# Kernel optimization log

Measured on AMD Instinct MI355X. Metric: run time of the kernel, lower is better.

Reference implementation:

```python
import jax, jax.numpy as jnp
import numpy as np

DIM = 96          # model dim (channels)
DS = 16           # d_state
K = 4             # d_conv
DIN = 2 * DIM     # d_inner = expand * dim
DTR = 6           # dt_rank = ceil(dim/16)
NSLICES = 4
B, H, W, Z = 2, 24, 24, 24
L = H * W * Z


def layernorm(x, g, b):
    mu = jnp.mean(x, -1, keepdims=True)
    var = jnp.var(x, -1, keepdims=True)
    return (x - mu) * jax.lax.rsqrt(var + 1e-5) * g + b


def dwconv_causal(x, w, b):
    # x: (B,L,Din), w: (Din,K) depthwise causal conv, b: (Din,)
    xt = x.swapaxes(1, 2)  # (B,Din,L)
    y = jax.lax.conv_general_dilated(xt, w[:, None, :], (1,), [(K - 1, 0)],
                                     feature_group_count=w.shape[0])
    return (y + b[None, :, None]).swapaxes(1, 2)


def selective_scan(u, dt, Bc, Cc, A, Dp):
    # u,dt: (B,L,Din); Bc,Cc: (B,L,DS); A: (Din,DS); Dp: (Din,)
    def step(h, inp):
        u_t, dt_t, B_t, C_t = inp
        dA = jnp.exp(dt_t[..., None] * A)                       # (B,Din,DS)
        h = dA * h + (dt_t * u_t)[..., None] * B_t[:, None, :]  # (B,Din,DS)
        y = jnp.sum(h * C_t[:, None, :], -1)                    # (B,Din)
        return h, y
    h0 = jnp.zeros((u.shape[0], u.shape[2], A.shape[1]), u.dtype)
    xs = (u.swapaxes(0, 1), dt.swapaxes(0, 1), Bc.swapaxes(0, 1), Cc.swapaxes(0, 1))
    _, ys = jax.lax.scan(step, h0, xs)
    return ys.swapaxes(0, 1) + u * Dp


def conv3d(x, w, b):
    y = jax.lax.conv_general_dilated(x, w, (1, 1, 1), [(1, 1), (1, 1), (1, 1)],
                                     dimension_numbers=('NCDHW', 'OIDHW', 'NCDHW'))
    return y + b[None, :, None, None, None]


def _slice_perm(t):  # group tokens by residue mod NSLICES (inter-slice scan)
    b, l, d = t.shape
    return t.reshape(b, l // NSLICES, NSLICES, d).transpose(0, 2, 1, 3).reshape(b, l, d)


def _slice_inv(t):
    b, l, d = t.shape
    return t.reshape(b, NSLICES, l // NSLICES, d).transpose(0, 2, 1, 3).reshape(b, l, d)


def setup_inputs() -> dict:
    key = jax.random.key(0)
    ks = jax.random.split(key, 10)
    r = lambda k, shp, s=0.02: jax.random.normal(k, shp, jnp.float32) * s
    return {
        'x': jax.random.normal(ks[0], (B, DIM, H, W, Z), jnp.float32),
        'ln_g': jnp.ones((DIM,), jnp.float32),
        'ln_b': jnp.zeros((DIM,), jnp.float32),
        'in_proj_w': r(ks[1], (2 * DIN, DIM)),
        'conv_w': r(ks[2], (3, DIN, K), 0.1),
        'conv_b': jnp.zeros((3, DIN), jnp.float32),
        'xproj_w': r(ks[3], (3, DTR + 2 * DS, DIN)),
        'dt_w': r(ks[4], (3, DIN, DTR), 0.1),
        'dt_b': jnp.full((3, DIN), -2.0, jnp.float32),
        'A_log': jnp.tile(jnp.log(jnp.arange(1, DS + 1, dtype=jnp.float32))[None, None, :], (3, DIN, 1)),
        'Dp': jnp.ones((3, DIN), jnp.float32),
        'out_proj_w': r(ks[5], (DIM, DIN)),
        'f1_w': r(ks[6], (DIM, 2 * DIM, 3, 3, 3)),
        'f1_b': jnp.zeros((DIM,), jnp.float32),
        'f2_w': r(ks[7], (DIM, 2 * DIM, 3, 3, 3)),
        'f2_b': jnp.zeros((DIM,), jnp.float32),
    }


def _mfa_forward(x, ln_g, ln_b, in_proj_w, conv_w, conv_b, xproj_w, dt_w, dt_b,
                 A_log, Dp, out_proj_w, f1_w, f1_b, f2_w, f2_b):
    b, c, h, w, z = x.shape
    l = h * w * z
    x_flat = x.reshape(b, c, l).swapaxes(1, 2)            # (B,L,C)
    x_norm = layernorm(x_flat, ln_g, ln_b)
    xz = x_norm @ in_proj_w.T                              # (B,L,2*Din)
    xin, zg = jnp.split(xz, [DIN], axis=-1)
    gate = jax.nn.silu(zg)

    ident = lambda t: t
    flip = lambda t: t[:, ::-1]
    perms = [(ident, ident), (flip, flip), (_slice_perm, _slice_inv)]

    ys = []
    for i, (fwd_p, inv_p) in enumerate(perms):
        xb = fwd_p(xin)
        u = jax.nn.silu(dwconv_causal(xb, conv_w[i], conv_b[i]))
        xdbl = u @ xproj_w[i].T                            # (B,L,DTR+2*DS)
        dtr, Bc, Cc = jnp.split(xdbl, [DTR, DTR + DS], axis=-1)
        dt = jax.nn.softplus(dtr @ dt_w[i].T + dt_b[i])
        y = selective_scan(u, dt, Bc, Cc, -jnp.exp(A_log[i]), Dp[i])
        ys.append(inv_p(y) * gate)
    q, k, v = ys                                           # each (B,L,Din)
    out = (q + k + v) @ out_proj_w.T                       # (B,L,C)

    # channel cross-covariance attention (head dim of 1 squeezed out)
    attn = jax.nn.softmax(jnp.einsum('bld,ble->bde', q, k), -1)   # (B,Din,Din)
    out_a = jnp.einsum('bld,bed->ble', v, attn)                   # v @ attn^T, (B,L,Din)
    out_a = out_a.reshape(b, 2 * c, h, w, z)                      # torch .view semantics (row-major)
    out_a = conv3d(out_a, f1_w, f1_b)
    out_m = out.swapaxes(1, 2).reshape(b, c, h, w, z)
    out2 = conv3d(jnp.concatenate([out_a, out_m], axis=1), f2_w, f2_b)
    return out2 + x


def reference(x, ln_g, ln_b, in_proj_w, conv_w, conv_b, xproj_w, dt_w, dt_b,
              A_log, Dp, out_proj_w, f1_w, f1_b, f2_w, f2_b):
    return _mfa_forward(x, ln_g, ln_b, in_proj_w, conv_w, conv_b, xproj_w, dt_w,
                        dt_b, A_log, Dp, out_proj_w, f1_w, f1_b, f2_w, f2_b)
```

## Files before the change

### kernel.cpp

```cpp
#include <hip/hip_runtime.h>
#include <hip/hip_bf16.h>
#include <math.h>

#define BB 2
#define C0 96
#define LTOT 13824
#define DINC 192
#define L4S 3456
#define NCHUNK 216
#define CLEN 64

#define WS_FLOATS 92000000
__device__ __attribute__((aligned(256))) float g_ws[WS_FLOATS];

typedef __bf16 bf16x8 __attribute__((ext_vector_type(8)));
typedef short  s16x8  __attribute__((ext_vector_type(8)));
typedef short  s16x4  __attribute__((ext_vector_type(4)));
typedef float  f32x4  __attribute__((ext_vector_type(4)));

__device__ __forceinline__ f32x4 mfma16(s16x8 a, s16x8 b, f32x4 c){
  return __builtin_amdgcn_mfma_f32_16x16x32_bf16(
      __builtin_bit_cast(bf16x8, a), __builtin_bit_cast(bf16x8, b), c, 0, 0, 0);
}

__device__ __forceinline__ int sigma_idx(int dir, int p){
  if (dir == 0) return p;
  if (dir == 1) return LTOT - 1 - p;
  return 4*(p % L4S) + (p / L4S);
}

__device__ __forceinline__ float silu_f(float x){
  return x / (1.f + __expf(-x));
}

__device__ __forceinline__ float softplus_f(float x){
  return (x > 20.f) ? x : __logf(1.f + __expf(x));
}

__device__ __forceinline__ short bf16r(float x){
  return (short)__builtin_bit_cast(unsigned short, __float2bfloat16(x));
}

__device__ __forceinline__ void pow_tree(float e1, float* pw){
  pw[0] = e1;
  pw[1] = e1*e1;
  pw[2] = pw[1]*e1;
  pw[3] = pw[1]*pw[1];
  pw[4] = pw[3]*e1;
  pw[5] = pw[3]*pw[1];
  pw[6] = pw[3]*pw[2];
  pw[7] = pw[3]*pw[3];
  pw[8] = pw[7]*e1;
  pw[9] = pw[7]*pw[1];
  pw[10]= pw[7]*pw[2];
  pw[11]= pw[7]*pw[3];
  pw[12]= pw[7]*pw[4];
  pw[13]= pw[7]*pw[5];
  pw[14]= pw[7]*pw[6];
  pw[15]= pw[7]*pw[7];
}

__global__ __launch_bounds__(256) void k_ln(const float* __restrict__ x,
    const float* __restrict__ g, const float* __restrict__ bt, float* __restrict__ xn)
{
  int i = blockIdx.x*256 + threadIdx.x;
  if (i >= BB*LTOT) return;
  int b = i / LTOT, ll = i % LTOT;
  const float* xp = x + (size_t)b*C0*LTOT + ll;
  float s = 0.f, ss = 0.f;
  for (int c = 0; c < C0; ++c){ float v = xp[(size_t)c*LTOT]; s += v; ss += v*v; }
  float mu = s * (1.f/C0);
  float var = ss * (1.f/C0) - mu*mu;
  float inv = rsqrtf(var + 1e-5f);
  float* op = xn + (size_t)i*C0;
  for (int c = 0; c < C0; ++c){
    float v = xp[(size_t)c*LTOT];
    op[c] = (v - mu)*inv*g[c] + bt[c];
  }
}

__global__ __launch_bounds__(256) void k_inproj(const float* __restrict__ xnorm,
    const float* __restrict__ W, float* __restrict__ xin, float* __restrict__ gate)
{
  __shared__ short Qs[256][40];
  __shared__ short Ws[96][40];
  int tid = threadIdx.x;
  long row0 = (long)blockIdx.x * 256;
  int y = blockIdx.y;
  int colb = (y & 1)*96;
  bool isGate = (y >= 2);
  const float* Wp = W + (long)y*96*96;
  int lane = tid & 63, wid = tid >> 6;
  int lr = lane & 15, lk = lane >> 4;
  f32x4 acc[4][6];
  #pragma unroll
  for (int i = 0; i < 4; ++i)
    #pragma unroll
    for (int j = 0; j < 6; ++j) acc[i][j] = f32x4{0.f,0.f,0.f,0.f};
  for (int kc = 0; kc < 3; ++kc){
    #pragma unroll
    for (int i = 0; i < 8; ++i){
      int flat4 = i*256 + tid;
      int row = flat4 >> 3, col4 = flat4 & 7;
      f32x4 a = *(const f32x4*)(xnorm + (row0 + row)*96 + kc*32 + col4*4);
      s16x4 o;
      #pragma unroll
      for (int e = 0; e < 4; ++e) o[e] = bf16r(a[e]);
      *(s16x4*)&Qs[row][col4*4] = o;
    }
    #pragma unroll
    for (int i = 0; i < 3; ++i){
      int flat4 = i*256 + tid;
      int row = flat4 >> 3, col4 = flat4 & 7;
      f32x4 wv = *(const f32x4*)(Wp + (long)row*96 + kc*32 + col4*4);
      s16x4 o;
      #pragma unroll
      for (int e = 0; e < 4; ++e) o[e] = bf16r(wv[e]);
      *(s16x4*)&Ws[row][col4*4] = o;
    }
    __syncthreads();
    #pragma unroll
    for (int rf = 0; rf < 4; ++rf){
      s16x8 af = *(const s16x8*)&Qs[wid*64 + rf*16 + lr][lk*8];
      #pragma unroll
      for (int cf = 0; cf < 6; ++cf){
        s16x8 wf = *(const s16x8*)&Ws[cf*16 + lr][lk*8];
        acc[rf][cf] = mfma16(wf, af, acc[rf][cf]);
      }
    }
    __syncthreads();
  }
  float* dst = isGate ? gate : xin;
  #pragma unroll
  for (int rf = 0; rf < 4; ++rf)
    #pragma unroll
    for (int cf = 0; cf < 6; ++cf){
      long l = row0 + wid*64 + rf*16 + lr;
      int n0 = cf*16 + lk*4;
      f32x4 v = acc[rf][cf];
      if (isGate){
        #pragma unroll
        for (int e = 0; e < 4; ++e) v[e] = silu_f(v[e]);
      }
      *(f32x4*)(dst + l*DINC + colb + n0) = v;
    }
}

__global__ __launch_bounds__(256) void k_xproj(const float* __restrict__ u,
    const float* __restrict__ W, float* __restrict__ xdbl)
{
  __shared__ short Qs[256][40];
  __shared__ short Ws[48][40];
  int tid = threadIdx.x;
  long row0 = (long)blockIdx.x * 256;
  int dir = (int)(row0 / 27648);
  const float* Wp = W + (long)dir*38*192;
  int lane = tid & 63, wid = tid >> 6;
  int lr = lane & 15, lk = lane >> 4;
  f32x4 acc[4][3];
  #pragma unroll
  for (int i = 0; i < 4; ++i)
    #pragma unroll
    for (int j = 0; j < 3; ++j) acc[i][j] = f32x4{0.f,0.f,0.f,0.f};
  for (int kc = 0; kc < 6; ++kc){
    #pragma unroll
    for (int i = 0; i < 8; ++i){
      int flat4 = i*256 + tid;
      int row = flat4 >> 3, col4 = flat4 & 7;
      f32x4 a = *(const f32x4*)(u + (row0 + row)*(long)DINC + kc*32 + col4*4);
      s16x4 o;
      #pragma unroll
      for (int e = 0; e < 4; ++e) o[e] = bf16r(a[e]);
      *(s16x4*)&Qs[row][col4*4] = o;
    }
    #pragma unroll
    for (int i = 0; i < 2; ++i){
      int flat4 = i*256 + tid;
      if (flat4 < 384){
        int row = flat4 >> 3, col4 = flat4 & 7;
        s16x4 o = {0,0,0,0};
        if (row < 38){
          f32x4 wv = *(const f32x4*)(Wp + (long)row*DINC + kc*32 + col4*4);
          #pragma unroll
          for (int e = 0; e < 4; ++e) o[e] = bf16r(wv[e]);
        }
        *(s16x4*)&Ws[row][col4*4] = o;
      }
    }
    __syncthreads();
    #pragma unroll
    for (int rf = 0; rf < 4; ++rf){
      s16x8 af = *(const s16x8*)&Qs[wid*64 + rf*16 + lr][lk*8];
      #pragma unroll
      for (int cf = 0; cf < 3; ++cf){
        s16x8 wf = *(const s16x8*)&Ws[cf*16 + lr][lk*8];
        acc[rf][cf] = mfma16(wf, af, acc[rf][cf]);
      }
    }
    __syncthreads();
  }
  #pragma unroll
  for (int rf = 0; rf < 4; ++rf)
    #pragma unroll
    for (int cf = 0; cf < 3; ++cf){
      long row = row0 + wid*64 + rf*16 + lr;
      int n0 = cf*16 + lk*4;
      if (n0 < 38)
        *(f32x4*)(xdbl + row*40 + n0) = acc[rf][cf];
    }
}

__global__ __launch_bounds__(256) void k_dwconv(const float* __restrict__ xin,
    const float* __restrict__ cw, const float* __restrict__ cb, float* __restrict__ u)
{
  long i = (long)blockIdx.x*256 + threadIdx.x;
  if (i >= 3L*BB*LTOT*48) return;
  int dq = (int)(i % 48); long t = i / 48;
  int p = (int)(t % LTOT); t /= LTOT;
  int b = (int)(t % BB); int dir = (int)(t / BB);
  int d0 = dq*4;
  f32x4 acc = *(const f32x4*)(cb + dir*DINC + d0);
  const float* wbase = cw + ((long)dir*DINC + d0)*4;
  f32x4 w0 = *(const f32x4*)(wbase);
  f32x4 w1 = *(const f32x4*)(wbase + 4);
  f32x4 w2 = *(const f32x4*)(wbase + 8);
  f32x4 w3 = *(const f32x4*)(wbase + 12);
  #pragma unroll
  for (int kk = 0; kk < 4; ++kk){
    int pp = p - 3 + kk;
    if (pp >= 0){
      int l = sigma_idx(dir, pp);
      f32x4 xv = *(const f32x4*)(xin + ((long)b*LTOT + l)*DINC + d0);
      acc[0] += xv[0] * w0[kk];
      acc[1] += xv[1] * w1[kk];
      acc[2] += xv[2] * w2[kk];
      acc[3] += xv[3] * w3[kk];
    }
  }
  #pragma unroll
  for (int e = 0; e < 4; ++e) acc[e] = silu_f(acc[e]);
  *(f32x4*)(u + (((long)dir*BB + b)*LTOT + p)*DINC + d0) = acc;
}

__global__ __launch_bounds__(256) void k_prepA(const float* __restrict__ al, float* __restrict__ A){
  int i = blockIdx.x*256 + threadIdx.x;
  if (i < 3*DINC*16) A[i] = -__expf(al[i]);
}

__global__ __launch_bounds__(192) void k_scan1(const float* __restrict__ u,
    const float* __restrict__ dt_w, const float* __restrict__ dt_b,
    const float* __restrict__ xdbl,
    const float* __restrict__ Abuf, float* __restrict__ aprod, float* __restrict__ hend)
{
  int d = threadIdx.x;
  int c  = blockIdx.x % NCHUNK;
  int bd = blockIdx.x / NCHUNK;
  int dir = bd >> 1;
  long pbase = (long)bd*LTOT + (long)c*CLEN;
  float w6[6];
  #pragma unroll
  for (int i = 0; i < 6; ++i) w6[i] = dt_w[(dir*DINC + d)*6 + i];
  float bdt = dt_b[dir*DINC + d];
  float A[16], h[16];
  #pragma unroll
  for (int s = 0; s < 16; ++s){
    A[s] = Abuf[((long)dir*DINC + d)*16 + s];
    h[s] = 0.f;
  }
  float A0 = A[0];
  bool fast = true;
  #pragma unroll
  for (int s = 1; s < 16; ++s)
    fast = fast && (fabsf(A[s] - (float)(s+1)*A0) <= 1e-4f*(float)(s+1));
  float sum_dt = 0.f;
  if (fast){
    for (int j = 0; j < CLEN; ++j){
      const float* xr = xdbl + (pbase + j)*40;
      float lu = u[(pbase + j)*DINC + d];
      float xv = bdt;
      #pragma unroll
      for (int i = 0; i < 6; ++i) xv += xr[i]*w6[i];
      float ldt = softplus_f(xv);
      sum_dt += ldt;
      float du = ldt*lu;
      float pw[16];
      pow_tree(__expf(ldt*A0), pw);
      #pragma unroll
      for (int s = 0; s < 16; ++s) h[s] = pw[s]*h[s] + du*xr[6+s];
    }
  } else {
    for (int j = 0; j < CLEN; ++j){
      const float* xr = xdbl + (pbase + j)*40;
      float lu = u[(pbase + j)*DINC + d];
      float xv = bdt;
      #pragma unroll
      for (int i = 0; i < 6; ++i) xv += xr[i]*w6[i];
      float ldt = softplus_f(xv);
      sum_dt += ldt;
      float du = ldt*lu;
      #pragma unroll
      for (int s = 0; s < 16; ++s) h[s] = __expf(ldt*A[s])*h[s] + du*xr[6+s];
    }
  }
  long oi = (((long)bd*DINC + d)*NCHUNK + c)*16;
  if (fast){
    float pw[16];
    pow_tree(__expf(A0*sum_dt), pw);
    #pragma unroll
    for (int s = 0; s < 16; ++s){ aprod[oi + s] = pw[s]; hend[oi + s] = h[s]; }
  } else {
    #pragma unroll
    for (int s = 0; s < 16; ++s){ aprod[oi + s] = __expf(A[s]*sum_dt); hend[oi + s] = h[s]; }
  }
}

__global__ __launch_bounds__(256) void k_scan2(float* __restrict__ aprod, const float* __restrict__ hend){
  long i = (long)blockIdx.x*256 + threadIdx.x;
  if (i >= 6L*DINC*16) return;
  int s = (int)(i & 15); long t = i >> 4;
  int d = (int)(t % DINC); int bd = (int)(t / DINC);
  long base = (((long)bd*DINC + d)*NCHUNK)*16 + s;
  float H = 0.f;
  for (int c = 0; c < NCHUNK; ++c){
    long idx = base + (long)c*16;
    float a = aprod[idx], he = hend[idx];
    aprod[idx] = H;
    H = he + a*H;
  }
}

__global__ __launch_bounds__(192) void k_scan3(const float* __restrict__ u,
    const float* __restrict__ dt_w, const float* __restrict__ dt_b,
    const float* __restrict__ xdbl,
    const float* __restrict__ Abuf, const float* __restrict__ hin,
    const float* __restrict__ Dp, const float* __restrict__ gate, float* __restrict__ qkv)
{
  int d = threadIdx.x;
  int c  = blockIdx.x % NCHUNK;
  int bd = blockIdx.x / NCHUNK;
  int dir = bd >> 1, b = bd & 1;
  long pbase = (long)bd*LTOT + (long)c*CLEN;
  float w6[6];
  #pragma unroll
  for (int i = 0; i < 6; ++i) w6[i] = dt_w[(dir*DINC + d)*6 + i];
  float bdt = dt_b[dir*DINC + d];
  float A[16], h[16];
  long oi = (((long)bd*DINC + d)*NCHUNK + c)*16;
  #pragma unroll
  for (int s = 0; s < 16; ++s){
    A[s] = Abuf[((long)dir*DINC + d)*16 + s];
    h[s] = hin[oi + s];
  }
  float A0 = A[0];
  bool fast = true;
  #pragma unroll
  for (int s = 1; s < 16; ++s)
    fast = fast && (fabsf(A[s] - (float)(s+1)*A0) <= 1e-4f*(float)(s+1));
  float Dv = Dp[dir*DINC + d];
  if (fast){
    for (int j = 0; j < CLEN; ++j){
      const float* xr = xdbl + (pbase + j)*40;
      float lu = u[(pbase + j)*DINC + d];
      float xv = bdt;
      #pragma unroll
      for (int i = 0; i < 6; ++i) xv += xr[i]*w6[i];
      float ldt = softplus_f(xv);
      float du = ldt*lu;
      float pw[16];
      pow_tree(__expf(ldt*A0), pw);
      float y = 0.f;
      #pragma unroll
      for (int s = 0; s < 16; ++s){
        h[s] = pw[s]*h[s] + du*xr[6+s];
        y += h[s]*xr[22+s];
      }
      int pl = c*CLEN + j;
      int l = sigma_idx(dir, pl);
      long li = (long)b*LTOT + l;
      qkv[(((long)dir*BB + b)*LTOT + l)*DINC + d] = (y + lu*Dv) * gate[li*DINC + d];
    }
  } else {
    for (int j = 0; j < CLEN; ++j){
      const float* xr = xdbl + (pbase + j)*40;
      float lu = u[(pbase + j)*DINC + d];
      float xv = bdt;
      #pragma unroll
      for (int i = 0; i < 6; ++i) xv += xr[i]*w6[i];
      float ldt = softplus_f(xv);
      float du = ldt*lu;
      float y = 0.f;
      #pragma unroll
      for (int s = 0; s < 16; ++s){
        h[s] = __expf(ldt*A[s])*h[s] + du*xr[6+s];
        y += h[s]*xr[22+s];
      }
      int pl = c*CLEN + j;
      int l = sigma_idx(dir, pl);
      long li = (long)b*LTOT + l;
      qkv[(((long)dir*BB + b)*LTOT + l)*DINC + d] = (y + lu*Dv) * gate[li*DINC + d];
    }
  }
}

__global__ __launch_bounds__(256) void k_zero(float* __restrict__ p, int n){
  int i = blockIdx.x*256 + threadIdx.x;
  if (i < n) p[i] = 0.f;
}

__global__ __launch_bounds__(256) void k_qk(const float* __restrict__ q,
    const float* __restrict__ k, float* __restrict__ attn)
{
  __shared__ float Qs[32][64];
  __shared__ float Ks[32][64];
  int tid = threadIdx.x;
  int bx = blockIdx.x;
  int lc = bx % 24; int et = (bx/24) % 3; int dtl = (bx/72) % 3; int b = bx/216;
  long base = (long)b*LTOT;
  int l0 = lc*576;
  float acc[4][4] = {};
  int col = tid & 63, rbase = tid >> 6;
  for (int ls = 0; ls < 576; ls += 32){
    #pragma unroll
    for (int rr = 0; rr < 8; ++rr){
      int r = rbase + rr*4;
      long l = base + l0 + ls + r;
      Qs[r][col] = q[l*DINC + dtl*64 + col];
      Ks[r][col] = k[l*DINC + et *64 + col];
    }
    __syncthreads();
    int d0 = (tid & 15)*4, e0 = (tid >> 4)*4;
    #pragma unroll
    for (int ll = 0; ll < 32; ++ll){
      float qa[4], ka[4];
      #pragma unroll
      for (int i = 0; i < 4; ++i){ qa[i] = Qs[ll][d0+i]; ka[i] = Ks[ll][e0+i]; }
      #pragma unroll
      for (int i = 0; i < 4; ++i)
        #pragma unroll
        for (int j = 0; j < 4; ++j) acc[i][j] += qa[i]*ka[j];
    }
    __syncthreads();
  }
  int d0 = (tid & 15)*4, e0 = (tid >> 4)*4;
  #pragma unroll
  for (int i = 0; i < 4; ++i)
    #pragma unroll
    for (int j = 0; j < 4; ++j)
      atomicAdd(&attn[((long)b*DINC + dtl*64 + d0 + i)*DINC + et*64 + e0 + j], acc[i][j]);
}

__global__ __launch_bounds__(64) void k_softmax(float* __restrict__ attn){
  int row = blockIdx.x, tid = threadIdx.x;
  float* p = attn + (long)row*DINC;
  float v0 = p[tid], v1 = p[tid+64], v2 = p[tid+128];
  float m = fmaxf(v0, fmaxf(v1, v2));
  #pragma unroll
  for (int off = 32; off >= 1; off >>= 1) m = fmaxf(m, __shfl_xor(m, off));
  float e0 = __expf(v0-m), e1 = __expf(v1-m), e2 = __expf(v2-m);
  float s = e0 + e1 + e2;
  #pragma unroll
  for (int off = 32; off >= 1; off >>= 1) s += __shfl_xor(s, off);
  float inv = 1.f/s;
  p[tid] = e0*inv; p[tid+64] = e1*inv; p[tid+128] = e2*inv;
}

__global__ __launch_bounds__(256) void k_outa(const float* __restrict__ v,
    const float* __restrict__ attn, __hip_bfloat16* __restrict__ inT1)
{
  __shared__ short Vs[192][40];
  __shared__ short Ws[192][40];
  int tid = threadIdx.x;
  int r0 = blockIdx.x;
  int b  = blockIdx.y;
  int lane = tid & 63, wid = tid >> 6;
  int lr = lane & 15, lk = lane >> 4;
  const float* vb = v + (long)b*LTOT*DINC;
  const float* ab = attn + (long)b*DINC*DINC;
  f32x4 acc[3][12];
  #pragma unroll
  for (int i = 0; i < 3; ++i)
    #pragma unroll
    for (int j = 0; j < 12; ++j) acc[i][j] = f32x4{0.f,0.f,0.f,0.f};
  for (int kc = 0; kc < 6; ++kc){
    #pragma unroll
    for (int i = 0; i < 6; ++i){
      int flat4 = i*256 + tid;
      int row = flat4 >> 3, col4 = flat4 & 7;
      int l = r0 + 72*row;
      f32x4 vv = *(const f32x4*)(vb + (long)l*DINC + kc*32 + col4*4);
      f32x4 aa = *(const f32x4*)(ab + (long)row*DINC + kc*32 + col4*4);
      s16x4 vs, as;
      #pragma unroll
      for (int e = 0; e < 4; ++e){ vs[e] = bf16r(vv[e]); as[e] = bf16r(aa[e]); }
      *(s16x4*)&Vs[row][col4*4] = vs;
      *(s16x4*)&Ws[row][col4*4] = as;
    }
    __syncthreads();
    #pragma unroll
    for (int cf = 0; cf < 12; ++cf){
      s16x8 wf = *(const s16x8*)&Ws[cf*16 + lr][lk*8];
      #pragma unroll
      for (int c = 0; c < 3; ++c){
        s16x8 af = *(const s16x8*)&Vs[wid*48 + c*16 + lr][lk*8];
        acc[c][cf] = mfma16(af, wf, acc[c][cf]);
      }
    }
    __syncthreads();
  }
  #pragma unroll
  for (int c = 0; c < 3; ++c)
    #pragma unroll
    for (int cf = 0; cf < 12; ++cf){
      int ch0 = wid*48 + c*16 + lk*4;
      int d = cf*16 + lr;
      s16x4 o;
      #pragma unroll
      for (int e = 0; e < 4; ++e) o[e] = bf16r(acc[c][cf][e]);
      *(s16x4*)(inT1 + ((long)(b*13824 + 192*r0 + d))*192 + ch0) = o;
    }
}

__global__ __launch_bounds__(256) void k_outm(const float* __restrict__ qkv,
    const float* __restrict__ Wo, __hip_bfloat16* __restrict__ inT2)
{
  __shared__ short Qs[256][40];
  __shared__ short Ws[96][40];
  int tid = threadIdx.x;
  long row0 = (long)blockIdx.x * 256;
  int lane = tid & 63, wid = tid >> 6;
  int lr = lane & 15, lk = lane >> 4;
  const size_t S = (size_t)BB*LTOT*DINC;
  f32x4 acc[4][6];
  #pragma unroll
  for (int i = 0; i < 4; ++i)
    #pragma unroll
    for (int j = 0; j < 6; ++j) acc[i][j] = f32x4{0.f,0.f,0.f,0.f};
  for (int kc = 0; kc < 6; ++kc){
    #pragma unroll
    for (int i = 0; i < 8; ++i){
      int flat4 = i*256 + tid;
      int row = flat4 >> 3, col4 = flat4 & 7;
      long base = (row0 + row)*(long)DINC + kc*32 + col4*4;
      f32x4 a0 = *(const f32x4*)(qkv + base);
      f32x4 a1 = *(const f32x4*)(qkv + S + base);
      f32x4 a2 = *(const f32x4*)(qkv + 2*S + base);
      s16x4 o;
      #pragma unroll
      for (int e = 0; e < 4; ++e) o[e] = bf16r(a0[e] + a1[e] + a2[e]);
      *(s16x4*)&Qs[row][col4*4] = o;
    }
    #pragma unroll
    for (int i = 0; i < 3; ++i){
      int flat4 = i*256 + tid;
      int row = flat4 >> 3, col4 = flat4 & 7;
      f32x4 wv = *(const f32x4*)(Wo + (long)row*DINC + kc*32 + col4*4);
      s16x4 o;
      #pragma unroll
      for (int e = 0; e < 4; ++e) o[e] = bf16r(wv[e]);
      *(s16x4*)&Ws[row][col4*4] = o;
    }
    __syncthreads();
    #pragma unroll
    for (int rf = 0; rf < 4; ++rf){
      s16x8 af = *(const s16x8*)&Qs[wid*64 + rf*16 + lr][lk*8];
      #pragma unroll
      for (int cf = 0; cf < 6; ++cf){
        s16x8 wf = *(const s16x8*)&Ws[cf*16 + lr][lk*8];
        acc[rf][cf] = mfma16(wf, af, acc[rf][cf]);
      }
    }
    __syncthreads();
  }
  #pragma unroll
  for (int rf = 0; rf < 4; ++rf)
    #pragma unroll
    for (int cf = 0; cf < 6; ++cf){
      long row = row0 + wid*64 + rf*16 + lr;
      int n0 = cf*16 + lk*4;
      s16x4 o;
      #pragma unroll
      for (int e = 0; e < 4; ++e) o[e] = bf16r(acc[rf][cf][e]);
      *(s16x4*)(inT2 + row*192 + 96 + n0) = o;
    }
}

__global__ __launch_bounds__(256) void k_pack(const float* __restrict__ w1,
    const float* __restrict__ w2, __hip_bfloat16* __restrict__ p1, __hip_bfloat16* __restrict__ p2)
{
  int i = blockIdx.x*256 + threadIdx.x;
  if (i >= 2*497664) return;
  int which = i / 497664; int r = i % 497664;
  int icl = r & 31; int oc = (r >> 5) % 96; int kc = (r / 3072) % 6; int t = r / 18432;
  const float* w = which ? w2 : w1;
  float v = w[(long)oc*5184 + (kc*32 + icl)*27 + t];
  (which ? p2 : p1)[r] = __float2bfloat16(v);
}

template<int CONV>
__global__ __launch_bounds__(128, 2) void k_convm(const __hip_bfloat16* __restrict__ inT,
    const __hip_bfloat16* __restrict__ Wp, float* __restrict__ pbuf)
{
  __shared__ short As[2][64][32];
  __shared__ short Ws[2][96][32];
  int tid = threadIdx.x;
  int bx = blockIdx.x;
  int g = bx / 432; int rem = bx % 432; int b = rem / 216; int tile = rem % 216;
  int sp0 = tile * 64;
  int kd = g - 1;
  int lane = tid & 63, wid = tid >> 6;
  int lr = lane & 15, lk = lane >> 4;
  const s16x8 zer = {0,0,0,0,0,0,0,0};

  int chnk = tid & 3;
  int hh[2], wwv[2], zzv[2], spv[2];
  #pragma unroll
  for (int k = 0; k < 2; ++k){
    int sp = sp0 + (tid >> 2) + 32*k;
    spv[k] = sp; hh[k] = sp/576; wwv[k] = (sp/24)%24; zzv[k] = sp%24;
  }

  f32x4 acc[6][2];
  #pragma unroll
  for (int i = 0; i < 6; ++i)
    #pragma unroll
    for (int j = 0; j < 2; ++j) acc[i][j] = f32x4{0.f,0.f,0.f,0.f};

  s16x8 av[2], wv[3];
  {
    int dw = -1, dz = -1;
    #pragma unroll
    for (int k = 0; k < 2; ++k){
      av[k] = zer;
      bool ok = ((unsigned)(hh[k]+kd) < 24u) && ((unsigned)(wwv[k]+dw) < 24u) && ((unsigned)(zzv[k]+dz) < 24u);
      if (ok){
        int spp = spv[k] + kd*576 + dw*24 + dz;
        av[k] = *(const s16x8*)(inT + ((long)(b*13824 + spp))*192 + chnk*8);
      }
    }
    long wb = ((long)(g*9)*6)*3072;
    #pragma unroll
    for (int k = 0; k < 3; ++k)
      wv[k] = *(const s16x8*)(Wp + wb + (long)(tid + 128*k)*8);
  }
  #pragma unroll
  for (int k = 0; k < 2; ++k)
    *(s16x8*)&As[0][(tid>>2) + 32*k][chnk*8] = av[k];
  #pragma unroll
  for (int k = 0; k < 3; ++k)
    *(s16x8*)&Ws[0][(tid + 128*k) >> 2][chnk*8] = wv[k];
  __syncthreads();

  for (int s = 0; s < 54; ++s){
    int buf = s & 1;
    int sn = s + 1;
    if (sn < 54){
      int t = sn / 6, kc = sn - 6*t;
      int td3 = t / 3;
      int dw = td3 - 1, dz = t - 3*td3 - 1;
      #pragma unroll
      for (int k = 0; k < 2; ++k){
        av[k] = zer;
        bool ok = ((unsigned)(hh[k]+kd) < 24u) && ((unsigned)(wwv[k]+dw) < 24u) && ((unsigned)(zzv[k]+dz) < 24u);
        if (ok){
          int spp = spv[k] + kd*576 + dw*24 + dz;
          av[k] = *(const s16x8*)(inT + ((long)(b*13824 + spp))*192 + kc*32 + chnk*8);
        }
      }
      long wb = ((long)(g*9 + t)*6 + kc)*3072;
      #pragma unroll
      for (int k = 0; k < 3; ++k)
        wv[k] = *(const s16x8*)(Wp + wb + (long)(tid + 128*k)*8);
    }
    s16x8 bfr[2];
    #pragma unroll
    for (int c = 0; c < 2; ++c)
      bfr[c] = *(const s16x8*)&As[buf][wid*32 + c*16 + lr][lk*8];
    #pragma unroll
    for (int cf = 0; cf < 6; ++cf){
      s16x8 wf = *(const s16x8*)&Ws[buf][cf*16 + lr][lk*8];
      #pragma unroll
      for (int c = 0; c < 2; ++c){
        if (CONV == 1) acc[cf][c] = mfma16(wf, bfr[c], acc[cf][c]);
        else           acc[cf][c] = mfma16(bfr[c], wf, acc[cf][c]);
      }
    }
    if (sn < 54){
      #pragma unroll
      for (int k = 0; k < 2; ++k)
        *(s16x8*)&As[buf^1][(tid>>2) + 32*k][chnk*8] = av[k];
      #pragma unroll
      for (int k = 0; k < 3; ++k)
        *(s16x8*)&Ws[buf^1][(tid + 128*k) >> 2][chnk*8] = wv[k];
    }
    __syncthreads();
  }

  long gb = (long)(g*2 + b);
  #pragma unroll
  for (int cf = 0; cf < 6; ++cf)
    #pragma unroll
    for (int c = 0; c < 2; ++c){
      if (CONV == 1){
        int sp = sp0 + wid*32 + c*16 + lr;
        int oc0 = cf*16 + lk*4;
        *reinterpret_cast<f32x4*>(pbuf + (gb*13824 + sp)*96 + oc0) = acc[cf][c];
      } else {
        int oc = cf*16 + lr;
        int spr = sp0 + wid*32 + c*16 + lk*4;
        *reinterpret_cast<f32x4*>(pbuf + (gb*96 + oc)*13824 + spr) = acc[cf][c];
      }
    }
}

__global__ __launch_bounds__(256) void k_red1(const float* __restrict__ pbuf,
    const float* __restrict__ bias, __hip_bfloat16* __restrict__ inT2)
{
  int i4 = blockIdx.x*256 + threadIdx.x;
  if (i4 >= 663552) return;
  int i = i4*4;
  int oc0 = i % 96;
  long row = i / 96;
  f32x4 v0 = *(const f32x4*)(pbuf + i);
  f32x4 v1 = *(const f32x4*)(pbuf + 2654208 + i);
  f32x4 v2 = *(const f32x4*)(pbuf + 2*2654208 + i);
  f32x4 bv = *(const f32x4*)(bias + oc0);
  s16x4 o;
  #pragma unroll
  for (int e = 0; e < 4; ++e) o[e] = bf16r(v0[e] + v1[e] + v2[e] + bv[e]);
  *(s16x4*)(inT2 + row*192 + oc0) = o;
}

__global__ __launch_bounds__(256) void k_red2(const float* __restrict__ pbuf,
    const float* __restrict__ bias, const float* __restrict__ x, float* __restrict__ out)
{
  int i4 = blockIdx.x*256 + threadIdx.x;
  if (i4 >= 663552) return;
  int i = i4*4;
  int oc = (i / 13824) % 96;
  f32x4 v0 = *(const f32x4*)(pbuf + i);
  f32x4 v1 = *(const f32x4*)(pbuf + 2654208 + i);
  f32x4 v2 = *(const f32x4*)(pbuf + 2*2654208 + i);
  f32x4 xv = *(const f32x4*)(x + i);
  f32x4 o;
  float bv = bias[oc];
  #pragma unroll
  for (int e = 0; e < 4; ++e) o[e] = v0[e] + v1[e] + v2[e] + bv + xv[e];
  *(f32x4*)(out + i) = o;
}

extern "C" void kernel_launch(void* const* d_in, const int* in_sizes, int n_in,
                              void* d_out, int out_size, void* d_ws, size_t ws_size,
                              hipStream_t stream)
{
  const float* x          = (const float*)d_in[0];
  const float* ln_g       = (const float*)d_in[1];
  const float* ln_b       = (const float*)d_in[2];
  const float* in_proj_w  = (const float*)d_in[3];
  const float* conv_w     = (const float*)d_in[4];
  const float* conv_b     = (const float*)d_in[5];
  const float* xproj_w    = (const float*)d_in[6];
  const float* dt_w       = (const float*)d_in[7];
  const float* dt_b       = (const float*)d_in[8];
  const float* A_log      = (const float*)d_in[9];
  const float* Dp         = (const float*)d_in[10];
  const float* out_proj_w = (const float*)d_in[11];
  const float* f1_w       = (const float*)d_in[12];
  const float* f1_b       = (const float*)d_in[13];
  const float* f2_w       = (const float*)d_in[14];
  const float* f2_b       = (const float*)d_in[15];
  float* out = (float*)d_out;

  const size_t BL = (size_t)BB*LTOT;
  const size_t S  = BL*DINC;

  void* wsp = nullptr;
  (void)hipGetSymbolAddress(&wsp, HIP_SYMBOL(g_ws));
  float* ws = (float*)wsp;
  size_t off = 0;
  auto alloc = [&](size_t n){ float* p = ws + off; off += n; return p; };
  float* xnorm = alloc(BL*C0);
  float* xin   = alloc(S);
  float* gate  = alloc(S);
  float* u     = alloc(3*S);
  float* xdbl  = alloc(3*BL*40);
  float* qkv   = alloc(3*S);
  float* Abuf  = alloc(3*DINC*16);
  float* aprod = alloc((size_t)6*DINC*16*NCHUNK);
  float* hend  = alloc((size_t)6*DINC*16*NCHUNK);
  float* attn  = alloc((size_t)BB*DINC*DINC);
  float* pbuf  = alloc((size_t)3*2654208);
  __hip_bfloat16* inT1 = (__hip_bfloat16*)alloc(2654208);
  __hip_bfloat16* inT2 = (__hip_bfloat16*)alloc(2654208);
  __hip_bfloat16* Wp1  = (__hip_bfloat16*)alloc(248832);
  __hip_bfloat16* Wp2  = (__hip_bfloat16*)alloc(248832);

  k_pack<<<3888, 256, 0, stream>>>(f1_w, f2_w, Wp1, Wp2);
  k_ln<<<108, 256, 0, stream>>>(x, ln_g, ln_b, xnorm);
  k_inproj<<<dim3(108, 4), 256, 0, stream>>>(xnorm, in_proj_w, xin, gate);
  k_dwconv<<<15552, 256, 0, stream>>>(xin, conv_w, conv_b, u);
  k_xproj<<<324, 256, 0, stream>>>(u, xproj_w, xdbl);
  k_prepA<<<36, 256, 0, stream>>>(A_log, Abuf);
  k_scan1<<<6*NCHUNK, 192, 0, stream>>>(u, dt_w, dt_b, xdbl, Abuf, aprod, hend);
  k_scan2<<<72, 256, 0, stream>>>(aprod, hend);
  k_scan3<<<6*NCHUNK, 192, 0, stream>>>(u, dt_w, dt_b, xdbl, Abuf, aprod, Dp, gate, qkv);
  k_zero<<<288, 256, 0, stream>>>(attn, BB*DINC*DINC);
  k_qk<<<432, 256, 0, stream>>>(qkv, qkv + S, attn);
  k_softmax<<<BB*DINC, 64, 0, stream>>>(attn);
  k_outa<<<dim3(72, 2), 256, 0, stream>>>(qkv + 2*S, attn, inT1);
  k_outm<<<108, 256, 0, stream>>>(qkv, out_proj_w, inT2);
  k_convm<1><<<1296, 128, 0, stream>>>(inT1, Wp1, pbuf);
  k_red1<<<2592, 256, 0, stream>>>(pbuf, f1_b, inT2);
  k_convm<2><<<1296, 128, 0, stream>>>(inT2, Wp2, pbuf);
  k_red2<<<2592, 256, 0, stream>>>(pbuf, f2_b, x, out);
}
```

Baseline: 447.0 us.

## Compute Q^T K with bf16 MFMA and deterministic partial-sum reduction

Replaces the scalar FP32 Q^T K accumulation kernel with one that stages Q and K transposed in shared memory as bf16 and uses 16x16x32 MFMA instructions. The atomicAdd accumulation and zeroing kernel are replaced by per-block partial tiles written to a scratch buffer and summed by a separate reduction kernel. This cuts ALU work and atomic contention but lowers the precision of the attention logits to bf16 inputs and adds an extra kernel launch plus scratch traffic.

```diff
diff --git a/kernel.cpp b/kernel.cpp
--- a/kernel.cpp
+++ b/kernel.cpp
@@ -402,51 +402,70 @@
   }
 }
 
-__global__ __launch_bounds__(256) void k_zero(float* __restrict__ p, int n){
-  int i = blockIdx.x*256 + threadIdx.x;
-  if (i < n) p[i] = 0.f;
-}
-
-__global__ __launch_bounds__(256) void k_qk(const float* __restrict__ q,
-    const float* __restrict__ k, float* __restrict__ attn)
-{
-  __shared__ float Qs[32][64];
-  __shared__ float Ks[32][64];
+__global__ __launch_bounds__(256) void k_qkm(const float* __restrict__ q,
+    const float* __restrict__ kkv, float* __restrict__ pb)
+{
+  __shared__ short Qst[64][36];
+  __shared__ short Kst[64][36];
   int tid = threadIdx.x;
   int bx = blockIdx.x;
   int lc = bx % 24; int et = (bx/24) % 3; int dtl = (bx/72) % 3; int b = bx/216;
-  long base = (long)b*LTOT;
-  int l0 = lc*576;
-  float acc[4][4] = {};
-  int col = tid & 63, rbase = tid >> 6;
-  for (int ls = 0; ls < 576; ls += 32){
-    #pragma unroll
-    for (int rr = 0; rr < 8; ++rr){
-      int r = rbase + rr*4;
-      long l = base + l0 + ls + r;
-      Qs[r][col] = q[l*DINC + dtl*64 + col];
-      Ks[r][col] = k[l*DINC + et *64 + col];
-    }
-    __syncthreads();
-    int d0 = (tid & 15)*4, e0 = (tid >> 4)*4;
-    #pragma unroll
-    for (int ll = 0; ll < 32; ++ll){
-      float qa[4], ka[4];
-      #pragma unroll
-      for (int i = 0; i < 4; ++i){ qa[i] = Qs[ll][d0+i]; ka[i] = Ks[ll][e0+i]; }
-      #pragma unroll
-      for (int i = 0; i < 4; ++i)
-        #pragma unroll
-        for (int j = 0; j < 4; ++j) acc[i][j] += qa[i]*ka[j];
-    }
-    __syncthreads();
-  }
-  int d0 = (tid & 15)*4, e0 = (tid >> 4)*4;
-  #pragma unroll
-  for (int i = 0; i < 4; ++i)
-    #pragma unroll
-    for (int j = 0; j < 4; ++j)
-      atomicAdd(&attn[((long)b*DINC + dtl*64 + d0 + i)*DINC + et*64 + e0 + j], acc[i][j]);
+  long base = (long)b*LTOT + (long)lc*576;
+  int lane = tid & 63, wid = tid >> 6;
+  int lr = lane & 15, lk = lane >> 4;
+  f32x4 acc[4];
+  #pragma unroll
+  for (int i = 0; i < 4; ++i) acc[i] = f32x4{0.f,0.f,0.f,0.f};
+  for (int sc = 0; sc < 18; ++sc){
+    int l0 = sc*32;
+    #pragma unroll
+    for (int i = 0; i < 2; ++i){
+      int flat4 = i*256 + tid;
+      int l = flat4 >> 4, dq = flat4 & 15;
+      int d0 = dq*4;
+      f32x4 qv = *(const f32x4*)(q   + (base + l0 + l)*(long)DINC + dtl*64 + d0);
+      f32x4 kv = *(const f32x4*)(kkv + (base + l0 + l)*(long)DINC + et *64 + d0);
+      #pragma unroll
+      for (int e = 0; e < 4; ++e){
+        Qst[d0+e][l] = bf16r(qv[e]);
+        Kst[d0+e][l] = bf16r(kv[e]);
+      }
+    }
+    __syncthreads();
+    s16x8 kf = *(const s16x8*)&Kst[wid*16 + lr][lk*8];
+    #pragma unroll
+    for (int rf = 0; rf < 4; ++rf){
+      s16x8 qf = *(const s16x8*)&Qst[rf*16 + lr][lk*8];
+      acc[rf] = mfma16(qf, kf, acc[rf]);
+    }
+    __syncthreads();
+  }
+  float* pbb = pb + (long)bx*4096;
+  #pragma unroll
+  for (int rf = 0; rf < 4; ++rf)
+    #pragma unroll
+    for (int e = 0; e < 4; ++e)
+      pbb[(rf*16 + lk*4 + e)*64 + wid*16 + lr] = acc[rf][e];
+}
+
+__global__ __launch_bounds__(256) void k_qred(const float* __restrict__ pb,
+    float* __restrict__ attn)
+{
+  int i4 = blockIdx.x*256 + threadIdx.x;
+  if (i4 >= 18432) return;
+  int i = i4*4;
+  int b = i / 36864; int r = i % 36864;
+  int dg = r / 192, eg = r % 192;
+  int dtl = dg / 64, d = dg % 64;
+  int et = eg / 64, e0 = eg % 64;
+  long pbase = ((long)(24*et + 72*dtl + 216*b))*4096 + d*64 + e0;
+  f32x4 s = {0.f,0.f,0.f,0.f};
+  for (int lc = 0; lc < 24; ++lc){
+    f32x4 v = *(const f32x4*)(pb + pbase + (long)lc*4096);
+    #pragma unroll
+    for (int e = 0; e < 4; ++e) s[e] += v[e];
+  }
+  *(f32x4*)(attn + i) = s;
 }
 
 __global__ __launch_bounds__(64) void k_softmax(float* __restrict__ attn){
@@ -803,8 +822,8 @@
   k_scan1<<<6*NCHUNK, 192, 0, stream>>>(u, dt_w, dt_b, xdbl, Abuf, aprod, hend);
   k_scan2<<<72, 256, 0, stream>>>(aprod, hend);
   k_scan3<<<6*NCHUNK, 192, 0, stream>>>(u, dt_w, dt_b, xdbl, Abuf, aprod, Dp, gate, qkv);
-  k_zero<<<288, 256, 0, stream>>>(attn, BB*DINC*DINC);
-  k_qk<<<432, 256, 0, stream>>>(qkv, qkv + S, attn);
+  k_qkm<<<432, 256, 0, stream>>>(qkv, qkv + S, pbuf);
+  k_qred<<<72, 256, 0, stream>>>(pbuf, attn);
   k_softmax<<<BB*DINC, 64, 0, stream>>>(attn);
   k_outa<<<dim3(72, 2), 256, 0, stream>>>(qkv + 2*S, attn, inT1);
   k_outm<<<108, 256, 0, stream>>>(qkv, out_proj_w, inT2);
```

Result: faster. 412.1 us (median of 3 runs) (-7.8%).
